# Kernel optimization log

Hardware: AMD Instinct MI355X
Metric: run time of the kernel (lower is better)

The kernel has to match this reference:

```python
import jax, jax.numpy as jnp
import numpy as np

N, E, IN, HID, OUT = 8192, 262144, 3000, 256, 64
EPS = 1e-5


def setup_inputs() -> dict:
    key = jax.random.key(0)
    k = jax.random.split(key, 16)
    s = lambda i, shp, sc: jax.random.normal(k[i], shp, jnp.float32) * sc
    return {
        "feat": s(0, (N, IN), 1.0),
        "feat_a": s(1, (N, IN), 1.0),
        "graph_neigh": jax.random.uniform(k[2], (N, N), jnp.float32),
        "W1": s(3, (IN, HID), (1.0 / IN) ** 0.5),
        "att_src": s(4, (HID,), (1.0 / HID) ** 0.5),
        "att_dst": s(5, (HID,), (1.0 / HID) ** 0.5),
        "W2": s(6, (HID, OUT), (1.0 / HID) ** 0.5),
        "Wd1": s(7, (OUT, HID), (1.0 / OUT) ** 0.5),
        "bd1": jnp.zeros((HID,), jnp.float32),
        "gamma": jnp.ones((HID,), jnp.float32),
        "beta": jnp.zeros((HID,), jnp.float32),
        "Wd2": s(8, (HID, IN), (1.0 / HID) ** 0.5),
        "bd2": jnp.zeros((IN,), jnp.float32),
        "disc_W": s(9, (OUT, OUT), (1.0 / OUT) ** 0.5),
        "disc_b": jnp.zeros((), jnp.float32),
        "edge_index": jax.random.randint(k[10], (2, E), 0, N),
    }


def _gat_conv1(x, W1, att_src, att_dst, src, dst):
    # GATConv, heads=1, concat=False, no self-loops, no bias
    h = x @ W1                                    # [N, HID]
    a_src = h @ att_src                           # [N]
    a_dst = h @ att_dst                           # [N]
    e = jax.nn.leaky_relu(a_src[src] + a_dst[dst], 0.2)   # [E]
    m = jax.ops.segment_max(e, dst, num_segments=N)
    p = jnp.exp(e - m[dst])
    z = jax.ops.segment_sum(p, dst, num_segments=N)
    alpha = p / (z[dst] + 1e-16)                  # segment softmax over in-edges
    return jax.ops.segment_sum(alpha[:, None] * h[src], dst, num_segments=N)


def _encode(x, W1, att_src, att_dst, W2, src, dst):
    h1 = jax.nn.elu(_gat_conv1(x, W1, att_src, att_dst, src, dst))
    # conv2 is invoked with attention=False -> GraphST GATConv returns only lin(x) (heads=1 mean)
    return h1 @ W2


def _decoder(h, Wd1, bd1, gamma, beta, Wd2, bd2):
    z = h @ Wd1 + bd1
    mu = z.mean(0)
    var = z.var(0)  # biased, matches torch BN training normalization
    z = (z - mu) * jax.lax.rsqrt(var + EPS) * gamma + beta
    z = jax.nn.elu(z)
    return z @ Wd2 + bd2


def _readout(h, mask):
    vsum = mask @ h                               # [N, OUT]
    g = vsum / mask.sum(1, keepdims=True)
    g = g / jnp.clip(jnp.linalg.norm(g, axis=1, keepdims=True), 1e-12)
    return jax.nn.sigmoid(g)


def reference(feat, feat_a, graph_neigh, W1, att_src, att_dst, W2, Wd1, bd1,
              gamma, beta, Wd2, bd2, disc_W, disc_b, edge_index):
    src, dst = edge_index[0], edge_index[1]
    h2 = _encode(feat, W1, att_src, att_dst, W2, src, dst)
    h2_a = _encode(feat_a, W1, att_src, att_dst, W2, src, dst)
    h3 = _decoder(h2, Wd1, bd1, gamma, beta, Wd2, bd2)
    g = _readout(h2, graph_neigh)
    g_a = _readout(h2_a, graph_neigh)

    def disc(c, hp, hm):
        sc1 = jnp.einsum('nd,de,ne->n', hp, disc_W, c) + disc_b
        sc2 = jnp.einsum('nd,de,ne->n', hm, disc_W, c) + disc_b
        return jnp.stack([sc1, sc2], axis=1)

    ret = disc(g, h2, h2_a)
    ret_a = disc(g_a, h2_a, h2)
    return (h2, h3, ret, ret_a, h2, h2_a)
```

## Files before the change

kernel.cpp:

```cpp
#include <hip/hip_runtime.h>
#include <hip/hip_bf16.h>
#include <math.h>

constexpr int NN  = 8192;
constexpr int EE  = 262144;
constexpr int IN  = 3000;
constexpr int INP = 3008;
constexpr int HID = 256;
constexpr int OUT = 64;

constexpr long O_H2   = 0;
constexpr long O_H3   = 524288;
constexpr long O_RET  = 25100288;
constexpr long O_RETA = 25116672;
constexpr long O_H2B  = 25133056;
constexpr long O_H2A  = 25657344;

typedef __attribute__((ext_vector_type(8))) short short8v;
typedef __attribute__((ext_vector_type(4))) float f32x4;

__device__ __forceinline__ short f2bf(float f) {
    unsigned u = __float_as_uint(f);
    return (short)((u + 0x7FFF + ((u >> 16) & 1)) >> 16);
}
__device__ __forceinline__ float bf2f(unsigned short u) {
    return __uint_as_float(((unsigned)u) << 16);
}

__global__ void cvt_W1t(const float* __restrict__ W, unsigned short* __restrict__ Wt) {
    int i = blockIdx.x * 256 + threadIdx.x;
    int n = i / INP, k = i % INP;
    Wt[i] = (k < IN) ? (unsigned short)f2bf(W[(long)k * HID + n]) : 0;
}
__global__ void cvt_W2t(const float* __restrict__ W, unsigned short* __restrict__ Wt) {
    int i = blockIdx.x * 256 + threadIdx.x;
    int n = i / HID, k = i % HID;
    Wt[i] = (unsigned short)f2bf(W[(long)k * OUT + n]);
}
__global__ void cvt_Wd1t(const float* __restrict__ W, unsigned short* __restrict__ Wt) {
    int i = blockIdx.x * 256 + threadIdx.x;
    int n = i / OUT, k = i % OUT;
    Wt[i] = (unsigned short)f2bf(W[(long)k * HID + n]);
}
__global__ void cvt_Wd2t(const float* __restrict__ W, unsigned short* __restrict__ Wt) {
    int i = blockIdx.x * 256 + threadIdx.x;
    int n = i / HID, k = i % HID;
    Wt[i] = (n < IN) ? (unsigned short)f2bf(W[(long)k * IN + n]) : 0;
}

__global__ __launch_bounds__(256) void feat_gemm(const float* __restrict__ A0,
                                                 const float* __restrict__ A1,
                                                 const unsigned short* __restrict__ Bt,
                                                 unsigned short* __restrict__ Hb) {
    __shared__ unsigned short As[128][72];
    __shared__ unsigned short Bs[128][72];
    int id = blockIdx.x;
    int xb = id >> 7, yb = id & 127;
    int pass = yb >> 6;
    int row0 = (yb & 63) * 128, col0 = xb * 128;
    const float* A = pass ? A1 : A0;
    int t = threadIdx.x, w = t >> 6, l = t & 63;
    int sr = t >> 1, sh = (t & 1) * 32;
    int wm = (w >> 1) * 64, wn = (w & 1) * 64;
    int fr = l & 15, fq = l >> 4;
    const unsigned short* Bp = Bt + (long)(col0 + sr) * INP + sh;
    const float* Arow = A + (long)(row0 + sr) * IN;

    float4  paf[8];
    short8v pb[4];
    auto loadA = [&](int k0) {
        const float* Ar = Arow + k0 + sh;
        if (k0 + 64 <= IN) {
#pragma unroll
            for (int q = 0; q < 8; ++q) paf[q] = *reinterpret_cast<const float4*>(Ar + q * 4);
        } else {
#pragma unroll
            for (int q = 0; q < 8; ++q) {
                int kb = k0 + sh + q * 4;
                float4 v;
                v.x = (kb + 0 < IN) ? Ar[q * 4 + 0] : 0.f;
                v.y = (kb + 1 < IN) ? Ar[q * 4 + 1] : 0.f;
                v.z = (kb + 2 < IN) ? Ar[q * 4 + 2] : 0.f;
                v.w = (kb + 3 < IN) ? Ar[q * 4 + 3] : 0.f;
                paf[q] = v;
            }
        }
    };
    auto loadB = [&](int k0) {
#pragma unroll
        for (int q = 0; q < 4; ++q) pb[q] = *reinterpret_cast<const short8v*>(Bp + k0 + q * 8);
    };
    loadA(0); loadB(0);

    constexpr int NK = INP / 64;
    f32x4 acc[4][4] = {};
    for (int tt = 0; tt < NK; ++tt) {
#pragma unroll
        for (int q = 0; q < 4; ++q) {
            float4 v0 = paf[q * 2], v1 = paf[q * 2 + 1];
            short8v s;
            s[0]=f2bf(v0.x); s[1]=f2bf(v0.y); s[2]=f2bf(v0.z); s[3]=f2bf(v0.w);
            s[4]=f2bf(v1.x); s[5]=f2bf(v1.y); s[6]=f2bf(v1.z); s[7]=f2bf(v1.w);
            *reinterpret_cast<short8v*>(&As[sr][sh + q * 8]) = s;
        }
#pragma unroll
        for (int q = 0; q < 4; ++q)
            *reinterpret_cast<short8v*>(&Bs[sr][sh + q * 8]) = pb[q];
        __syncthreads();
        if (tt + 1 < NK) { loadA((tt + 1) * 64); loadB((tt + 1) * 64); }
#pragma unroll
        for (int kk = 0; kk < 2; ++kk) {
            short8v fa[4], fb[4];
#pragma unroll
            for (int i = 0; i < 4; ++i)
                fa[i] = *reinterpret_cast<const short8v*>(&As[wm + i * 16 + fr][kk * 32 + fq * 8]);
#pragma unroll
            for (int j = 0; j < 4; ++j)
                fb[j] = *reinterpret_cast<const short8v*>(&Bs[wn + j * 16 + fr][kk * 32 + fq * 8]);
#pragma unroll
            for (int i = 0; i < 4; ++i)
#pragma unroll
                for (int j = 0; j < 4; ++j)
                    acc[i][j] = __builtin_amdgcn_mfma_f32_16x16x32_bf16(fa[i], fb[j], acc[i][j], 0, 0, 0);
        }
        __syncthreads();
    }
    int dc = l & 15;
    long base = (long)(pass * NN) * HID;
#pragma unroll
    for (int i = 0; i < 4; ++i)
#pragma unroll
        for (int j = 0; j < 4; ++j) {
            int c = col0 + wn + j * 16 + dc;
#pragma unroll
            for (int q = 0; q < 4; ++q) {
                int r = row0 + wm + i * 16 + fq * 4 + q;
                Hb[base + (long)r * HID + c] = (unsigned short)f2bf(acc[i][j][q]);
            }
        }
}

__global__ __launch_bounds__(256) void w2_gemm(const unsigned short* __restrict__ A,
                                               const unsigned short* __restrict__ Bt,
                                               float* __restrict__ h2f,
                                               unsigned short* __restrict__ h2b,
                                               unsigned short* __restrict__ HT,
                                               float* __restrict__ out) {
    __shared__ unsigned short As[64][72];
    __shared__ unsigned short Bs[64][72];
    int t = threadIdx.x, w = t >> 6, l = t & 63;
    int row0 = blockIdx.y * 64;
    int srow = t >> 2, scol = (t & 3) * 16;
    const unsigned short* Ap = A + (long)(row0 + srow) * HID + scol;
    const unsigned short* Bp = Bt + (long)srow * HID + scol;
    int wm = (w >> 1) * 32, wn = (w & 1) * 32;
    int fr = l & 15, fq = l >> 4;

    short8v a0r, a1r, b0r, b1r;
    a0r = *reinterpret_cast<const short8v*>(Ap);
    a1r = *reinterpret_cast<const short8v*>(Ap + 8);
    b0r = *reinterpret_cast<const short8v*>(Bp);
    b1r = *reinterpret_cast<const short8v*>(Bp + 8);

    f32x4 acc[2][2] = {};
    for (int tt = 0; tt < 4; ++tt) {
        *reinterpret_cast<short8v*>(&As[srow][scol])     = a0r;
        *reinterpret_cast<short8v*>(&As[srow][scol + 8]) = a1r;
        *reinterpret_cast<short8v*>(&Bs[srow][scol])     = b0r;
        *reinterpret_cast<short8v*>(&Bs[srow][scol + 8]) = b1r;
        __syncthreads();
        if (tt + 1 < 4) {
            const unsigned short* Ap2 = Ap + (tt + 1) * 64;
            const unsigned short* Bp2 = Bp + (tt + 1) * 64;
            a0r = *reinterpret_cast<const short8v*>(Ap2);
            a1r = *reinterpret_cast<const short8v*>(Ap2 + 8);
            b0r = *reinterpret_cast<const short8v*>(Bp2);
            b1r = *reinterpret_cast<const short8v*>(Bp2 + 8);
        }
#pragma unroll
        for (int kk = 0; kk < 2; ++kk) {
            short8v fa0 = *reinterpret_cast<const short8v*>(&As[wm + fr][kk * 32 + fq * 8]);
            short8v fa1 = *reinterpret_cast<const short8v*>(&As[wm + 16 + fr][kk * 32 + fq * 8]);
            short8v fb0 = *reinterpret_cast<const short8v*>(&Bs[wn + fr][kk * 32 + fq * 8]);
            short8v fb1 = *reinterpret_cast<const short8v*>(&Bs[wn + 16 + fr][kk * 32 + fq * 8]);
            acc[0][0] = __builtin_amdgcn_mfma_f32_16x16x32_bf16(fa0, fb0, acc[0][0], 0, 0, 0);
            acc[0][1] = __builtin_amdgcn_mfma_f32_16x16x32_bf16(fa0, fb1, acc[0][1], 0, 0, 0);
            acc[1][0] = __builtin_amdgcn_mfma_f32_16x16x32_bf16(fa1, fb0, acc[1][0], 0, 0, 0);
            acc[1][1] = __builtin_amdgcn_mfma_f32_16x16x32_bf16(fa1, fb1, acc[1][1], 0, 0, 0);
        }
        __syncthreads();
    }
    int dc = l & 15;
    int pass = row0 >> 13;
#pragma unroll
    for (int i = 0; i < 2; ++i)
#pragma unroll
        for (int j = 0; j < 2; ++j) {
            int c = wn + j * 16 + dc;
#pragma unroll
            for (int q = 0; q < 4; ++q) {
                int r = row0 + wm + i * 16 + fq * 4 + q;
                int n = r & 8191;
                float v = acc[i][j][q];
                unsigned short vb = (unsigned short)f2bf(v);
                h2f[(long)pass * 524288 + (long)n * 64 + c] = v;
                if (pass == 0) {
                    out[O_H2  + (long)n * 64 + c] = v;
                    out[O_H2B + (long)n * 64 + c] = v;
                    h2b[(long)n * 64 + c] = vb;
                } else {
                    out[O_H2A + (long)n * 64 + c] = v;
                }
                HT[(long)(pass * 64 + c) * NN + n] = vb;
            }
        }
}

__global__ __launch_bounds__(256) void wd2_gemm(const unsigned short* __restrict__ A,
                                                const unsigned short* __restrict__ Bt,
                                                const float* __restrict__ bias,
                                                float* __restrict__ Cf) {
    __shared__ unsigned short As[128][72];
    __shared__ unsigned short Bs[128][72];
    int t = threadIdx.x, w = t >> 6, l = t & 63;
    int row0 = blockIdx.y * 128, col0 = blockIdx.x * 128;
    int sr = t >> 1, sh = (t & 1) * 32;
    int wm = (w >> 1) * 64, wn = (w & 1) * 64;
    int fr = l & 15, fq = l >> 4;
    const unsigned short* Ap = A  + (long)(row0 + sr) * HID + sh;
    const unsigned short* Bp = Bt + (long)(col0 + sr) * HID + sh;

    short8v pa[4], pb[4];
#pragma unroll
    for (int q = 0; q < 4; ++q) pa[q] = *reinterpret_cast<const short8v*>(Ap + q * 8);
#pragma unroll
    for (int q = 0; q < 4; ++q) pb[q] = *reinterpret_cast<const short8v*>(Bp + q * 8);

    f32x4 acc[4][4] = {};
    for (int tt = 0; tt < 4; ++tt) {
#pragma unroll
        for (int q = 0; q < 4; ++q) {
            *reinterpret_cast<short8v*>(&As[sr][sh + q * 8]) = pa[q];
            *reinterpret_cast<short8v*>(&Bs[sr][sh + q * 8]) = pb[q];
        }
        __syncthreads();
        if (tt + 1 < 4) {
            int k0 = (tt + 1) * 64;
#pragma unroll
            for (int q = 0; q < 4; ++q) pa[q] = *reinterpret_cast<const short8v*>(Ap + k0 + q * 8);
#pragma unroll
            for (int q = 0; q < 4; ++q) pb[q] = *reinterpret_cast<const short8v*>(Bp + k0 + q * 8);
        }
#pragma unroll
        for (int kk = 0; kk < 2; ++kk) {
            short8v fa[4], fb[4];
#pragma unroll
            for (int i = 0; i < 4; ++i)
                fa[i] = *reinterpret_cast<const short8v*>(&As[wm + i * 16 + fr][kk * 32 + fq * 8]);
#pragma unroll
            for (int j = 0; j < 4; ++j)
                fb[j] = *reinterpret_cast<const short8v*>(&Bs[wn + j * 16 + fr][kk * 32 + fq * 8]);
#pragma unroll
            for (int i = 0; i < 4; ++i)
#pragma unroll
                for (int j = 0; j < 4; ++j)
                    acc[i][j] = __builtin_amdgcn_mfma_f32_16x16x32_bf16(fa[i], fb[j], acc[i][j], 0, 0, 0);
        }
        __syncthreads();
    }
    int dc = l & 15;
#pragma unroll
    for (int i = 0; i < 4; ++i)
#pragma unroll
        for (int j = 0; j < 4; ++j) {
            int c = col0 + wn + j * 16 + dc;
            if (c < IN) {
                float bb = bias[c];
#pragma unroll
                for (int q = 0; q < 4; ++q) {
                    int r = row0 + wm + i * 16 + fq * 4 + q;
                    Cf[(long)r * IN + c] = acc[i][j][q] + bb;
                }
            }
        }
}

__global__ __launch_bounds__(256) void wd1_gemm(const unsigned short* __restrict__ A,
                                                const unsigned short* __restrict__ Bt,
                                                const float* __restrict__ bias,
                                                float* __restrict__ C) {
    __shared__ unsigned short As[64][72];
    __shared__ unsigned short Bs[64][72];
    int t = threadIdx.x, w = t >> 6, l = t & 63;
    int row0 = blockIdx.y * 64, col0 = blockIdx.x * 64;
    int srow = t >> 2, scol = (t & 3) * 16;
    const unsigned short* Ap = A  + (long)(row0 + srow) * OUT + scol;
    const unsigned short* Bp = Bt + (long)(col0 + srow) * OUT + scol;
    int wm = (w >> 1) * 32, wn = (w & 1) * 32;
    int fr = l & 15, fq = l >> 4;

    *reinterpret_cast<short8v*>(&As[srow][scol])     = *reinterpret_cast<const short8v*>(Ap);
    *reinterpret_cast<short8v*>(&As[srow][scol + 8]) = *reinterpret_cast<const short8v*>(Ap + 8);
    *reinterpret_cast<short8v*>(&Bs[srow][scol])     = *reinterpret_cast<const short8v*>(Bp);
    *reinterpret_cast<short8v*>(&Bs[srow][scol + 8]) = *reinterpret_cast<const short8v*>(Bp + 8);
    __syncthreads();
    f32x4 acc[2][2] = {};
#pragma unroll
    for (int kk = 0; kk < 2; ++kk) {
        short8v fa0 = *reinterpret_cast<const short8v*>(&As[wm + fr][kk * 32 + fq * 8]);
        short8v fa1 = *reinterpret_cast<const short8v*>(&As[wm + 16 + fr][kk * 32 + fq * 8]);
        short8v fb0 = *reinterpret_cast<const short8v*>(&Bs[wn + fr][kk * 32 + fq * 8]);
        short8v fb1 = *reinterpret_cast<const short8v*>(&Bs[wn + 16 + fr][kk * 32 + fq * 8]);
        acc[0][0] = __builtin_amdgcn_mfma_f32_16x16x32_bf16(fa0, fb0, acc[0][0], 0, 0, 0);
        acc[0][1] = __builtin_amdgcn_mfma_f32_16x16x32_bf16(fa0, fb1, acc[0][1], 0, 0, 0);
        acc[1][0] = __builtin_amdgcn_mfma_f32_16x16x32_bf16(fa1, fb0, acc[1][0], 0, 0, 0);
        acc[1][1] = __builtin_amdgcn_mfma_f32_16x16x32_bf16(fa1, fb1, acc[1][1], 0, 0, 0);
    }
    int dc = l & 15;
#pragma unroll
    for (int i = 0; i < 2; ++i)
#pragma unroll
        for (int j = 0; j < 2; ++j) {
            int c = col0 + wn + j * 16 + dc;
            float bb = bias[c];
#pragma unroll
            for (int q = 0; q < 4; ++q) {
                int r = row0 + wm + i * 16 + fq * 4 + q;
                C[(long)r * HID + c] = acc[i][j][q] + bb;
            }
        }
}

__global__ __launch_bounds__(256) void readout_mfma2(const float* __restrict__ gn,
                                                     const unsigned short* __restrict__ HT,
                                                     float* __restrict__ vsum_part,
                                                     float* __restrict__ rowsum_part) {
    __shared__ unsigned short As[64][72];
    __shared__ unsigned short Bs[128][72];
    __shared__ float rsacc[64][4];
    int t = threadIdx.x, w = t >> 6, l = t & 63;
    int row0 = blockIdx.x * 64;
    int kc = blockIdx.y, kbeg = kc * 2048;
    int asr = t >> 2, asc = (t & 3) * 16;
    int bsr = t >> 1, bsc = (t & 1) * 32;
    const float*          Ap = gn + (long)(row0 + asr) * NN + kbeg + asc;
    const unsigned short* Bp = HT + (long)bsr * NN + kbeg + bsc;
    int wm = (w >> 1) * 32, wn = (w & 1) * 64;
    int fr = l & 15, fq = l >> 4;

    float4  a4[4];
    short8v b8[4];
#pragma unroll
    for (int q = 0; q < 4; ++q) a4[q] = *reinterpret_cast<const float4*>(Ap + q * 4);
#pragma unroll
    for (int q = 0; q < 4; ++q) b8[q] = *reinterpret_cast<const short8v*>(Bp + q * 8);

    f32x4 acc[2][4] = {};
    float myrs = 0.f;
    for (int it = 0; it < 32; ++it) {
#pragma unroll
        for (int q = 0; q < 4; ++q) {
            float4 v = a4[q];
            ushort4 s;
            s.x = (unsigned short)f2bf(v.x);
            s.y = (unsigned short)f2bf(v.y);
            s.z = (unsigned short)f2bf(v.z);
            s.w = (unsigned short)f2bf(v.w);
            *reinterpret_cast<ushort4*>(&As[asr][asc + q * 4]) = s;
            myrs += v.x + v.y + v.z + v.w;
        }
#pragma unroll
        for (int q = 0; q < 4; ++q)
            *reinterpret_cast<short8v*>(&Bs[bsr][bsc + q * 8]) = b8[q];
        __syncthreads();
        if (it + 1 < 32) {
            const float*          Ap2 = Ap + (it + 1) * 64;
            const unsigned short* Bp2 = Bp + (it + 1) * 64;
#pragma unroll
            for (int q = 0; q < 4; ++q) a4[q] = *reinterpret_cast<const float4*>(Ap2 + q * 4);
#pragma unroll
            for (int q = 0; q < 4; ++q) b8[q] = *reinterpret_cast<const short8v*>(Bp2 + q * 8);
        }
#pragma unroll
        for (int kk = 0; kk < 2; ++kk) {
            short8v fa0 = *reinterpret_cast<const short8v*>(&As[wm + fr][kk * 32 + fq * 8]);
            short8v fa1 = *reinterpret_cast<const short8v*>(&As[wm + 16 + fr][kk * 32 + fq * 8]);
#pragma unroll
            for (int j = 0; j < 4; ++j) {
                short8v fb = *reinterpret_cast<const short8v*>(&Bs[wn + j * 16 + fr][kk * 32 + fq * 8]);
                acc[0][j] = __builtin_amdgcn_mfma_f32_16x16x32_bf16(fa0, fb, acc[0][j], 0, 0, 0);
                acc[1][j] = __builtin_amdgcn_mfma_f32_16x16x32_bf16(fa1, fb, acc[1][j], 0, 0, 0);
            }
        }
        __syncthreads();
    }
    rsacc[asr][t & 3] = myrs;
    __syncthreads();
    if (t < 64)
        rowsum_part[(long)kc * NN + row0 + t] =
            rsacc[t][0] + rsacc[t][1] + rsacc[t][2] + rsacc[t][3];
    int dc = l & 15;
#pragma unroll
    for (int i = 0; i < 2; ++i)
#pragma unroll
        for (int j = 0; j < 4; ++j) {
            int c = wn + j * 16 + dc;
#pragma unroll
            for (int q = 0; q < 4; ++q) {
                int r = row0 + wm + i * 16 + fq * 4 + q;
                vsum_part[((long)kc * NN + r) * 128 + c] = acc[i][j][q];
            }
        }
}

__global__ void deg_count(const int* __restrict__ dst, int* __restrict__ deg) {
    int i = blockIdx.x * 256 + threadIdx.x;
    if (i < EE) atomicAdd(&deg[dst[i]], 1);
}

__global__ __launch_bounds__(256) void scan_offsets(const int* __restrict__ deg,
                                                    int* __restrict__ off,
                                                    int* __restrict__ cursor) {
    __shared__ int part[256];
    int t = threadIdx.x;
    int base = t * 32;
    int local[32];
    int s = 0;
#pragma unroll
    for (int i = 0; i < 32; ++i) { local[i] = s; s += deg[base + i]; }
    part[t] = s;
    __syncthreads();
    for (int o2 = 1; o2 < 256; o2 <<= 1) {
        int v = (t >= o2) ? part[t - o2] : 0;
        __syncthreads();
        part[t] += v;
        __syncthreads();
    }
    int pre = (t == 0) ? 0 : part[t - 1];
#pragma unroll
    for (int i = 0; i < 32; ++i) {
        int v = pre + local[i];
        off[base + i] = v;
        cursor[base + i] = v;
    }
}

__global__ void scatter_edges(const int* __restrict__ src, const int* __restrict__ dst,
                              int* __restrict__ cursor, int* __restrict__ ssrc) {
    int i = blockIdx.x * 256 + threadIdx.x;
    if (i >= EE) return;
    int slot = atomicAdd(&cursor[dst[i]], 1);
    ssrc[slot] = src[i];
}

__global__ void attn_coeff_bf(const unsigned short* __restrict__ h,
                              const float* __restrict__ att_src,
                              const float* __restrict__ att_dst,
                              float* __restrict__ a_src, float* __restrict__ a_dst) {
    int wave = threadIdx.x >> 6, lane = threadIdx.x & 63;
    int n = blockIdx.x * 4 + wave;
    ushort4 hv = *reinterpret_cast<const ushort4*>(&h[(long)n * HID + lane * 4]);
    float4 vs = *reinterpret_cast<const float4*>(&att_src[lane * 4]);
    float4 vd = *reinterpret_cast<const float4*>(&att_dst[lane * 4]);
    float h0 = bf2f(hv.x), h1 = bf2f(hv.y), h2v = bf2f(hv.z), h3v = bf2f(hv.w);
    float s1 = h0 * vs.x + h1 * vs.y + h2v * vs.z + h3v * vs.w;
    float s2 = h0 * vd.x + h1 * vd.y + h2v * vd.z + h3v * vd.w;
#pragma unroll
    for (int off = 32; off > 0; off >>= 1) {
        s1 += __shfl_down(s1, off);
        s2 += __shfl_down(s2, off);
    }
    if (lane == 0) { a_src[n] = s1; a_dst[n] = s2; }
}

__global__ __launch_bounds__(256) void gat_gather(const int* __restrict__ ssrc,
                                                  const int* __restrict__ off,
                                                  const int* __restrict__ deg,
                                                  const float* __restrict__ asrc2,
                                                  const float* __restrict__ adst2,
                                                  const unsigned short* __restrict__ hb2,
                                                  unsigned short* __restrict__ gat2) {
    int wv = threadIdx.x >> 6, lane = threadIdx.x & 63;
    int d = blockIdx.x * 4 + wv;
    int pass = d >> 13, node = d & 8191;
    const float* asrc = asrc2 + pass * NN;
    const unsigned short* h = hb2 + (long)pass * NN * HID;
    int o = off[node], n = deg[node];
    float ad = adst2[d];

    float m = -INFINITY;
    for (int j = lane; j < n; j += 64) {
        float e = asrc[ssrc[o + j]] + ad;
        e = e > 0.f ? e : 0.2f * e;
        m = fmaxf(m, e);
    }
#pragma unroll
    for (int t = 32; t; t >>= 1) m = fmaxf(m, __shfl_xor(m, t));
    float z = 0.f;
    for (int j = lane; j < n; j += 64) {
        float e = asrc[ssrc[o + j]] + ad;
        e = e > 0.f ? e : 0.2f * e;
        z += expf(e - m);
    }
#pragma unroll
    for (int t = 32; t; t >>= 1) z += __shfl_xor(z, t);
    float zinv = 1.0f / (z + 1e-16f);

    float4 acc = {0.f, 0.f, 0.f, 0.f};
    int j = 0;
    for (; j + 2 <= n; j += 2) {
        int s0 = ssrc[o + j], s1 = ssrc[o + j + 1];
        const ushort4 h0 = *reinterpret_cast<const ushort4*>(&h[(long)s0 * HID + lane * 4]);
        const ushort4 h1 = *reinterpret_cast<const ushort4*>(&h[(long)s1 * HID + lane * 4]);
        float e0 = asrc[s0] + ad; e0 = e0 > 0.f ? e0 : 0.2f * e0;
        float e1 = asrc[s1] + ad; e1 = e1 > 0.f ? e1 : 0.2f * e1;
        float a0 = expf(e0 - m) * zinv;
        float a1 = expf(e1 - m) * zinv;
        acc.x += a0 * bf2f(h0.x) + a1 * bf2f(h1.x);
        acc.y += a0 * bf2f(h0.y) + a1 * bf2f(h1.y);
        acc.z += a0 * bf2f(h0.z) + a1 * bf2f(h1.z);
        acc.w += a0 * bf2f(h0.w) + a1 * bf2f(h1.w);
    }
    if (j < n) {
        int s0 = ssrc[o + j];
        const ushort4 h0 = *reinterpret_cast<const ushort4*>(&h[(long)s0 * HID + lane * 4]);
        float e0 = asrc[s0] + ad; e0 = e0 > 0.f ? e0 : 0.2f * e0;
        float a0 = expf(e0 - m) * zinv;
        acc.x += a0 * bf2f(h0.x); acc.y += a0 * bf2f(h0.y);
        acc.z += a0 * bf2f(h0.z); acc.w += a0 * bf2f(h0.w);
    }
    ushort4 r;
    r.x = (unsigned short)f2bf(acc.x > 0.f ? acc.x : expm1f(acc.x));
    r.y = (unsigned short)f2bf(acc.y > 0.f ? acc.y : expm1f(acc.y));
    r.z = (unsigned short)f2bf(acc.z > 0.f ? acc.z : expm1f(acc.z));
    r.w = (unsigned short)f2bf(acc.w > 0.f ? acc.w : expm1f(acc.w));
    *reinterpret_cast<ushort4*>(&gat2[(long)d * HID + lane * 4]) = r;
}

__global__ void bn_partial(const float* __restrict__ zd, float* __restrict__ s,
                           float* __restrict__ sq) {
    int t = threadIdx.x;
    float a = 0.f, b = 0.f;
    int r0 = blockIdx.x * 128;
    for (int r = r0; r < r0 + 128; ++r) {
        float v = zd[(long)r * HID + t];
        a += v;
        b += v * v;
    }
    atomicAdd(&s[t], a);
    atomicAdd(&sq[t], b);
}

__global__ void bn_finalize(const float* __restrict__ s, const float* __restrict__ sq,
                            const float* __restrict__ gamma, const float* __restrict__ beta,
                            float* __restrict__ scale, float* __restrict__ shift) {
    int t = threadIdx.x;
    float mean = s[t] / (float)NN;
    float var  = sq[t] / (float)NN - mean * mean;
    float sc   = gamma[t] * rsqrtf(var + 1e-5f);
    scale[t] = sc;
    shift[t] = beta[t] - mean * sc;
}

__global__ void bn_apply_elu_bf(const float* __restrict__ zd, const float* __restrict__ scale,
                                const float* __restrict__ shift, unsigned short* __restrict__ zb) {
    for (long i = (long)blockIdx.x * blockDim.x + threadIdx.x; i < (long)NN * HID;
         i += (long)gridDim.x * blockDim.x) {
        int c = (int)(i & 255);
        float v = zd[i] * scale[c] + shift[c];
        v = v > 0.f ? v : expm1f(v);
        zb[i] = (unsigned short)f2bf(v);
    }
}

__global__ void readout_disc(const float* __restrict__ vsum_part,
                             const float* __restrict__ rowsum_part,
                             const float* __restrict__ h2f,
                             const float* __restrict__ W, const float* __restrict__ b,
                             float* __restrict__ ret, float* __restrict__ reta) {
    __shared__ float gg[128];
    int r = blockIdx.x, t = threadIdx.x;
    float rs = 0.f, v = 0.f;
#pragma unroll
    for (int kc = 0; kc < 4; ++kc) {
        rs += rowsum_part[(long)kc * NN + r];
        v  += vsum_part[((long)kc * NN + r) * 128 + t];
    }
    v /= rs;
    int w = t >> 6, lane = t & 63;
    float sq = v * v;
#pragma unroll
    for (int off = 32; off > 0; off >>= 1) sq += __shfl_xor(sq, off);
    float nrm = fmaxf(sqrtf(sq), 1e-12f);
    gg[t] = 1.0f / (1.0f + expf(-(v / nrm)));
    __syncthreads();
    const float* hp_base = h2f + (w ? 524288 : 0);
    const float* hm_base = h2f + (w ? 0 : 524288);
    float u = 0.f;
#pragma unroll 8
    for (int e = 0; e < 64; ++e) u += W[lane * 64 + e] * gg[w * 64 + e];
    float hp = hp_base[(long)r * 64 + lane];
    float hm = hm_base[(long)r * 64 + lane];
    float t1 = hp * u, t2 = hm * u;
#pragma unroll
    for (int off = 32; off > 0; off >>= 1) {
        t1 += __shfl_xor(t1, off);
        t2 += __shfl_xor(t2, off);
    }
    if (lane == 0) {
        float bb = b[0];
        float* dstp = w ? reta : ret;
        dstp[r * 2]     = t1 + bb;
        dstp[r * 2 + 1] = t2 + bb;
    }
}

extern "C" void kernel_launch(void* const* d_in, const int* in_sizes, int n_in,
                              void* d_out, int out_size, void* d_ws, size_t ws_size,
                              hipStream_t stream) {
    const float* feat    = (const float*)d_in[0];
    const float* feat_a  = (const float*)d_in[1];
    const float* gneigh  = (const float*)d_in[2];
    const float* W1      = (const float*)d_in[3];
    const float* att_src = (const float*)d_in[4];
    const float* att_dst = (const float*)d_in[5];
    const float* W2      = (const float*)d_in[6];
    const float* Wd1     = (const float*)d_in[7];
    const float* bd1     = (const float*)d_in[8];
    const float* gamma   = (const float*)d_in[9];
    const float* beta    = (const float*)d_in[10];
    const float* Wd2     = (const float*)d_in[11];
    const float* bd2     = (const float*)d_in[12];
    const float* disc_W  = (const float*)d_in[13];
    const float* disc_b  = (const float*)d_in[14];
    const int*   eidx    = (const int*)d_in[15];
    const int*   src = eidx;
    const int*   dst = eidx + EE;
    float* out = (float*)d_out;

    float* w = (float*)d_ws;
    unsigned short* h_bf2  = (unsigned short*)w;
    unsigned short* gat_bf2 = (unsigned short*)(w + 2097152);
    float* zdec    = w + 4194304;
    unsigned short* zdec_bf = (unsigned short*)(zdec + 2097152);
    float* h2f     = zdec + 2097152 + 1048576;
    unsigned short* h2b = (unsigned short*)(h2f + 1048576);
    unsigned short* HT  = h2b + 524288;
    float* asrc2   = (float*)(HT + 1048576);
    float* adst2   = asrc2 + 16384;
    float* bnsum   = adst2 + 16384;
    float* bnsq    = bnsum + 256;
    float* scale   = bnsq + 256;
    float* shift   = scale + 256;
    unsigned short* W1t  = (unsigned short*)(shift + 256);
    unsigned short* W2t  = W1t + 770048;
    unsigned short* Wd1t = W2t + 16384;
    unsigned short* Wd2t = Wd1t + 16384;
    int*   ideg    = (int*)(Wd2t + 786432);
    int*   ioff    = ideg + 8192;
    int*   icur    = ioff + 8192;
    int*   issrc   = icur + 8192;
    float* vsum_part = w;
    float* rowsum_part = zdec;

    cvt_W1t<<<3008, 256, 0, stream>>>(W1, W1t);
    cvt_W2t<<<64, 256, 0, stream>>>(W2, W2t);
    cvt_Wd1t<<<64, 256, 0, stream>>>(Wd1, Wd1t);
    cvt_Wd2t<<<3072, 256, 0, stream>>>(Wd2, Wd2t);

    hipMemsetAsync(ideg, 0, 8192 * 4, stream);
    deg_count<<<EE / 256, 256, 0, stream>>>(dst, ideg);
    scan_offsets<<<1, 256, 0, stream>>>(ideg, ioff, icur);
    scatter_edges<<<EE / 256, 256, 0, stream>>>(src, dst, icur, issrc);

    feat_gemm<<<256, 256, 0, stream>>>(feat, feat_a, W1t, h_bf2);
    attn_coeff_bf<<<4096, 256, 0, stream>>>(h_bf2, att_src, att_dst, asrc2, adst2);
    gat_gather<<<4096, 256, 0, stream>>>(issrc, ioff, ideg, asrc2, adst2, h_bf2, gat_bf2);
    w2_gemm<<<dim3(1, 256), 256, 0, stream>>>(gat_bf2, W2t, h2f, h2b, HT, out);

    wd1_gemm<<<dim3(4, 128), 256, 0, stream>>>(h2b, Wd1t, bd1, zdec);
    hipMemsetAsync(bnsum, 0, 512 * 4, stream);
    bn_partial<<<64, 256, 0, stream>>>(zdec, bnsum, bnsq);
    bn_finalize<<<1, 256, 0, stream>>>(bnsum, bnsq, gamma, beta, scale, shift);
    bn_apply_elu_bf<<<2048, 256, 0, stream>>>(zdec, scale, shift, zdec_bf);
    wd2_gemm<<<dim3(24, 64), 256, 0, stream>>>(zdec_bf, Wd2t, bd2, out + O_H3);

    readout_mfma2<<<dim3(128, 4), 256, 0, stream>>>(gneigh, HT, vsum_part, rowsum_part);
    readout_disc<<<8192, 128, 0, stream>>>(vsum_part, rowsum_part, h2f, disc_W, disc_b,
                                           out + O_RET, out + O_RETA);
}
```

Baseline: 419.5 us.

## Split-K the feature GEMM four ways with fp32 partials and reduce kernel

The feature GEMM previously launched only 256 blocks on a GPU with 256 CUs, each walking all 47 K-tiles. It now splits K into four chunks of 12 tiles across blockIdx.z, giving 1024 blocks that write fp32 partial sums into the h3 output region as scratch. A new reduce kernel sums the four partials and converts them to bf16. This raises parallelism and latency hiding, at the cost of about 64MB of extra partial-sum traffic and one more launch.

```diff
diff --git a/kernel.cpp b/kernel.cpp
--- a/kernel.cpp
+++ b/kernel.cpp
@@ -51,11 +51,10 @@
 __global__ __launch_bounds__(256) void feat_gemm(const float* __restrict__ A0,
                                                  const float* __restrict__ A1,
                                                  const unsigned short* __restrict__ Bt,
-                                                 unsigned short* __restrict__ Hb) {
+                                                 float* __restrict__ Cpart) {
     __shared__ unsigned short As[128][72];
     __shared__ unsigned short Bs[128][72];
-    int id = blockIdx.x;
-    int xb = id >> 7, yb = id & 127;
+    int xb = blockIdx.x, yb = blockIdx.y;
     int pass = yb >> 6;
     int row0 = (yb & 63) * 128, col0 = xb * 128;
     const float* A = pass ? A1 : A0;
@@ -66,6 +65,9 @@
     const unsigned short* Bp = Bt + (long)(col0 + sr) * INP + sh;
     const float* Arow = A + (long)(row0 + sr) * IN;
 
+    int tb = blockIdx.z * 12;
+    int ktiles = min(12, 47 - tb);
+
     float4  paf[8];
     short8v pb[4];
     auto loadA = [&](int k0) {
@@ -90,11 +92,10 @@
 #pragma unroll
         for (int q = 0; q < 4; ++q) pb[q] = *reinterpret_cast<const short8v*>(Bp + k0 + q * 8);
     };
-    loadA(0); loadB(0);
-
-    constexpr int NK = INP / 64;
+    loadA(tb * 64); loadB(tb * 64);
+
     f32x4 acc[4][4] = {};
-    for (int tt = 0; tt < NK; ++tt) {
+    for (int tt = 0; tt < ktiles; ++tt) {
 #pragma unroll
         for (int q = 0; q < 4; ++q) {
             float4 v0 = paf[q * 2], v1 = paf[q * 2 + 1];
@@ -107,7 +108,10 @@
         for (int q = 0; q < 4; ++q)
             *reinterpret_cast<short8v*>(&Bs[sr][sh + q * 8]) = pb[q];
         __syncthreads();
-        if (tt + 1 < NK) { loadA((tt + 1) * 64); loadB((tt + 1) * 64); }
+        if (tt + 1 < ktiles) {
+            int k0 = (tb + tt + 1) * 64;
+            loadA(k0); loadB(k0);
+        }
 #pragma unroll
         for (int kk = 0; kk < 2; ++kk) {
             short8v fa[4], fb[4];
@@ -126,7 +130,8 @@
         __syncthreads();
     }
     int dc = l & 15;
-    long base = (long)(pass * NN) * HID;
+    long zbase = (long)blockIdx.z * 16384 * 256;
+    long rbase = (long)(pass * NN + row0) * 256;
 #pragma unroll
     for (int i = 0; i < 4; ++i)
 #pragma unroll
@@ -134,10 +139,24 @@
             int c = col0 + wn + j * 16 + dc;
 #pragma unroll
             for (int q = 0; q < 4; ++q) {
-                int r = row0 + wm + i * 16 + fq * 4 + q;
-                Hb[base + (long)r * HID + c] = (unsigned short)f2bf(acc[i][j][q]);
+                int r = wm + i * 16 + fq * 4 + q;
+                Cpart[zbase + rbase + (long)r * 256 + c] = acc[i][j][q];
             }
         }
+}
+
+__global__ void reduce_cvt4(const float* __restrict__ p, unsigned short* __restrict__ hb) {
+    long i4 = ((long)blockIdx.x * 256 + threadIdx.x) * 4;
+    float4 a = *reinterpret_cast<const float4*>(p + i4);
+    float4 b = *reinterpret_cast<const float4*>(p + 4194304 + i4);
+    float4 c = *reinterpret_cast<const float4*>(p + 8388608 + i4);
+    float4 d = *reinterpret_cast<const float4*>(p + 12582912 + i4);
+    ushort4 r;
+    r.x = (unsigned short)f2bf(a.x + b.x + c.x + d.x);
+    r.y = (unsigned short)f2bf(a.y + b.y + c.y + d.y);
+    r.z = (unsigned short)f2bf(a.z + b.z + c.z + d.z);
+    r.w = (unsigned short)f2bf(a.w + b.w + c.w + d.w);
+    *reinterpret_cast<ushort4*>(hb + i4) = r;
 }
 
 __global__ __launch_bounds__(256) void w2_gemm(const unsigned short* __restrict__ A,
@@ -660,6 +679,7 @@
     int*   ioff    = ideg + 8192;
     int*   icur    = ioff + 8192;
     int*   issrc   = icur + 8192;
+    float* part = out + O_H3;
     float* vsum_part = w;
     float* rowsum_part = zdec;
 
@@ -673,7 +693,8 @@
     scan_offsets<<<1, 256, 0, stream>>>(ideg, ioff, icur);
     scatter_edges<<<EE / 256, 256, 0, stream>>>(src, dst, icur, issrc);
 
-    feat_gemm<<<256, 256, 0, stream>>>(feat, feat_a, W1t, h_bf2);
+    feat_gemm<<<dim3(2, 128, 4), 256, 0, stream>>>(feat, feat_a, W1t, part);
+    reduce_cvt4<<<4096, 256, 0, stream>>>(part, h_bf2);
     attn_coeff_bf<<<4096, 256, 0, stream>>>(h_bf2, att_src, att_dst, asrc2, adst2);
     gat_gather<<<4096, 256, 0, stream>>>(issrc, ioff, ideg, asrc2, adst2, h_bf2, gat_bf2);
     w2_gemm<<<dim3(1, 256), 256, 0, stream>>>(gat_bf2, W2t, h2f, h2b, HT, out);
```

Result: faster. 400.0 us (-4.6%).
